# Optimization experiments

Hardware: AMD Instinct MI355X
Metric: run time of the kernel (lower is better)

## Reference

```python
import jax, jax.numpy as jnp
import numpy as np

NUM_GROUPS = 32
EPS = 1e-6


def group_norm(x, scale, bias):
    b, c, h, w = x.shape
    g = NUM_GROUPS
    xg = x.reshape(b, g, c // g, h, w)
    mean = jnp.mean(xg, axis=(2, 3, 4), keepdims=True)
    var = jnp.var(xg, axis=(2, 3, 4), keepdims=True)
    xg = (xg - mean) * jax.lax.rsqrt(var + EPS)
    x = xg.reshape(b, c, h, w)
    return x * scale[None, :, None, None] + bias[None, :, None, None]


def conv1x1(x, w, b):
    # x: [B,C,H,W], w: [Cout,Cin], b: [Cout]
    return jnp.einsum('bchw,oc->bohw', x, w) + b[None, :, None, None]


def setup_inputs() -> dict:
    key = jax.random.key(0)
    ks = jax.random.split(key, 11)
    C = 512
    B, H, W = 8, 64, 64
    s = 1.0 / np.sqrt(C)
    inp = {
        'x': jax.random.normal(ks[0], (B, C, H, W), jnp.float32),
        'gn_scale': jnp.ones((C,), jnp.float32),
        'gn_bias': jnp.zeros((C,), jnp.float32),
        'wq': jax.random.normal(ks[1], (C, C), jnp.float32) * s,
        'bq': jnp.zeros((C,), jnp.float32),
        'wk': jax.random.normal(ks[2], (C, C), jnp.float32) * s,
        'bk': jnp.zeros((C,), jnp.float32),
        'wv': jax.random.normal(ks[3], (C, C), jnp.float32) * s,
        'bv': jnp.zeros((C,), jnp.float32),
    }
    return inp


def reference(x, gn_scale, gn_bias, wq, bq, wk, bk, wv, bv):
    b, c, h, w = x.shape
    h_ = group_norm(x, gn_scale, gn_bias)
    q = conv1x1(h_, wq, bq).reshape(b, c, h * w)  # [b,c,n]
    k = conv1x1(h_, wk, bk).reshape(b, c, h * w)
    v = conv1x1(h_, wv, bv).reshape(b, c, h * w)
    scale = jnp.asarray(c, x.dtype) ** -0.5
    # attn[b,i,j] = sum_c q[b,c,i] * k[b,c,j]
    attn = jnp.einsum('bci,bcj->bij', q, k) * scale
    attn = jax.nn.softmax(attn, axis=2)  # softmax over j (keys)
    # A[b,c,i] = sum_j v[b,c,j] * attn[b,i,j]
    A = jnp.einsum('bcj,bij->bci', v, attn).reshape(b, c, h, w)
    return x + A
```

## Files before the change

kernel.cpp:

```cpp
#include <hip/hip_runtime.h>
#include <hip/hip_bf16.h>

#define B_   8
#define C_   512
#define N_   4096
#define G_   32
#define CPG  16
#define EPSV 1e-6f

typedef short s16x8 __attribute__((ext_vector_type(8)));
typedef float f32x4 __attribute__((ext_vector_type(4)));

__device__ __forceinline__ unsigned short f2bf(float f) {
    unsigned u = __builtin_bit_cast(unsigned, f);
    u += 0x7fffu + ((u >> 16) & 1u);
    return (unsigned short)(u >> 16);
}

__device__ __forceinline__ void gload_lds16(const unsigned short* g, unsigned short* l) {
    __builtin_amdgcn_global_load_lds((const __attribute__((address_space(1))) void*)g,
                                     (__attribute__((address_space(3))) void*)l, 16, 0, 0);
}

__global__ __launch_bounds__(256) void gn_stats_k(const float* __restrict__ x,
                                                  float* __restrict__ stats) {
    int blk = blockIdx.x;
    const float4* p = (const float4*)(x + (size_t)blk * (CPG * N_));
    float s = 0.f, ss = 0.f;
    for (int i = threadIdx.x; i < (CPG * N_) / 4; i += 256) {
        float4 v = p[i];
        s  += v.x + v.y + v.z + v.w;
        ss += v.x * v.x + v.y * v.y + v.z * v.z + v.w * v.w;
    }
    for (int off = 32; off > 0; off >>= 1) {
        s  += __shfl_down(s, off);
        ss += __shfl_down(ss, off);
    }
    __shared__ float r0[4], r1[4];
    int wid = threadIdx.x >> 6;
    if ((threadIdx.x & 63) == 0) { r0[wid] = s; r1[wid] = ss; }
    __syncthreads();
    if (threadIdx.x == 0) {
        s  = r0[0] + r0[1] + r0[2] + r0[3];
        ss = r1[0] + r1[1] + r1[2] + r1[3];
        const float inv = 1.0f / (CPG * N_);
        float mean = s * inv;
        float var  = ss * inv - mean * mean;
        stats[2 * blk]     = mean;
        stats[2 * blk + 1] = rsqrtf(var + EPSV);
    }
}

__global__ __launch_bounds__(256) void cvt_w_k(const float* __restrict__ wq,
                                               const float* __restrict__ wk,
                                               const float* __restrict__ wv,
                                               unsigned short* __restrict__ wbf) {
    int i = blockIdx.x * 256 + threadIdx.x;
    const int percc = C_ * C_ / 4;
    const float* src; int li;
    if (i < percc)            { src = wq; li = i; }
    else if (i < 2 * percc)   { src = wk; li = i - percc; }
    else                      { src = wv; li = i - 2 * percc; }
    float4 v = ((const float4*)src)[li];
    unsigned u0 = (unsigned)f2bf(v.x) | ((unsigned)f2bf(v.y) << 16);
    unsigned u1 = (unsigned)f2bf(v.z) | ((unsigned)f2bf(v.w) << 16);
    uint2 o; o.x = u0; o.y = u1;
    *(uint2*)&wbf[(size_t)i * 4] = o;
}

__global__ __launch_bounds__(256) void gn_apply_k(const float* __restrict__ x,
                                                  const float* __restrict__ stats,
                                                  const float* __restrict__ gsc,
                                                  const float* __restrict__ gbi,
                                                  unsigned short* __restrict__ h_t) {
    int nt = blockIdx.x, ct = blockIdx.y, b = blockIdx.z;
    int n0 = nt * 64, c0 = ct * 64;
    __shared__ unsigned short T[64][72];
    int t = threadIdx.x;
    int cl = t >> 2, ch = t & 3;
    int c = c0 + cl;
    int g = c >> 4;
    float mean = stats[(b * G_ + g) * 2];
    float rstd = stats[(b * G_ + g) * 2 + 1];
    float sc = gsc[c] * rstd;
    float bi = gbi[c] - mean * sc;
    const float* xr = x + (size_t)(b * C_ + c) * N_ + n0 + ch * 16;
    #pragma unroll
    for (int q = 0; q < 4; ++q) {
        float4 v = *(const float4*)(xr + q * 4);
        int nl = ch * 16 + q * 4;
        T[nl + 0][cl] = f2bf(fmaf(v.x, sc, bi));
        T[nl + 1][cl] = f2bf(fmaf(v.y, sc, bi));
        T[nl + 2][cl] = f2bf(fmaf(v.z, sc, bi));
        T[nl + 3][cl] = f2bf(fmaf(v.w, sc, bi));
    }
    __syncthreads();
    #pragma unroll
    for (int it = 0; it < 2; ++it) {
        int id = t + it * 256;
        int nl = id >> 3, part = id & 7;
        s16x8 val = *(const s16x8*)&T[nl][part * 8];
        *(s16x8*)&h_t[((size_t)b * N_ + n0 + nl) * C_ + c0 + part * 8] = val;
    }
}

__device__ __forceinline__ void gemm_core(const unsigned short* A, int ldA,
                                          const unsigned short* Bm, int ldB,
                                          unsigned short* Al, unsigned short* Bl,
                                          f32x4 (&acc)[4][4], int ksteps, int t) {
    int w = t >> 6, l = t & 63;
    int wm = (w >> 1) * 64, wn = (w & 1) * 64;
    int lr = l & 15, lg = l >> 4;
    int srow = w * 16 + (l >> 2);
    int sp   = (l & 3) * 8;

    #pragma unroll
    for (int it = 0; it < 2; ++it) {
        gload_lds16(&A [(size_t)(it * 64 + srow) * ldA + sp], &Al[it * 2048 + w * 512 + l * 8]);
        gload_lds16(&Bm[(size_t)(it * 64 + srow) * ldB + sp], &Bl[it * 2048 + w * 512 + l * 8]);
    }
    __syncthreads();

    int cur = 0;
    for (int s = 0; s < ksteps; ++s) {
        if (s + 1 < ksteps) {
            const unsigned short* ga = A  + (s + 1) * 32;
            const unsigned short* gb = Bm + (s + 1) * 32;
            int off = (cur ^ 1) * 4096;
            #pragma unroll
            for (int it = 0; it < 2; ++it) {
                gload_lds16(&ga[(size_t)(it * 64 + srow) * ldA + sp], &Al[off + it * 2048 + w * 512 + l * 8]);
                gload_lds16(&gb[(size_t)(it * 64 + srow) * ldB + sp], &Bl[off + it * 2048 + w * 512 + l * 8]);
            }
        }
        const unsigned short* la = Al + cur * 4096;
        const unsigned short* lb = Bl + cur * 4096;
        s16x8 a[4], b[4];
        #pragma unroll
        for (int i = 0; i < 4; ++i) a[i] = *(const s16x8*)&la[(wm + i * 16 + lr) * 32 + lg * 8];
        #pragma unroll
        for (int j = 0; j < 4; ++j) b[j] = *(const s16x8*)&lb[(wn + j * 16 + lr) * 32 + lg * 8];
        #pragma unroll
        for (int i = 0; i < 4; ++i)
            #pragma unroll
            for (int j = 0; j < 4; ++j)
                acc[i][j] = __builtin_amdgcn_mfma_f32_16x16x32_bf16(a[i], b[j], acc[i][j], 0, 0, 0);
        __syncthreads();
        cur ^= 1;
    }
}

__global__ __launch_bounds__(256, 4) void qkv_k(const unsigned short* __restrict__ h_t,
                                                const unsigned short* __restrict__ wbf,
                                                const float* __restrict__ bq,
                                                const float* __restrict__ bk,
                                                const float* __restrict__ bv,
                                                unsigned short* __restrict__ q_t,
                                                unsigned short* __restrict__ k_t,
                                                unsigned short* __restrict__ vv) {
    int which = blockIdx.z % 3;
    int b     = blockIdx.z / 3;
    int bx = blockIdx.x, by = blockIdx.y;
    const unsigned short* A;
    const unsigned short* Bm;
    unsigned short* Cm;
    const float* bias;
    int m0, n0; size_t ldc; bool biasRow;
    const unsigned short* hb = h_t + (size_t)b * N_ * C_;
    if (which < 2) {
        A = hb; Bm = wbf + (size_t)which * C_ * C_;
        Cm = (which == 0 ? q_t : k_t) + (size_t)b * N_ * C_;
        bias = (which == 0 ? bq : bk);
        m0 = bx * 128; n0 = by * 128; ldc = C_; biasRow = false;
    } else {
        A = wbf + (size_t)2 * C_ * C_; Bm = hb;
        Cm = vv + (size_t)b * C_ * N_;
        bias = bv;
        m0 = by * 128; n0 = bx * 128; ldc = N_; biasRow = true;
    }

    __shared__ char smem[35072];
    unsigned short* Al = (unsigned short*)smem;
    unsigned short* Bl = Al + 8192;
    unsigned short* El = (unsigned short*)smem;

    int t = threadIdx.x;
    int wid = t >> 6, lane = t & 63;
    int wm = (wid >> 1) * 64, wn = (wid & 1) * 64;
    int lr = lane & 15, lg = lane >> 4;

    f32x4 acc[4][4] = {};
    gemm_core(A + (size_t)m0 * C_, C_, Bm + (size_t)n0 * C_, C_, Al, Bl, acc, C_ / 32, t);

    float rb[4][4], cb[4];
    #pragma unroll
    for (int i = 0; i < 4; ++i)
        #pragma unroll
        for (int r = 0; r < 4; ++r)
            rb[i][r] = biasRow ? bias[m0 + wm + i * 16 + lg * 4 + r] : 0.f;
    #pragma unroll
    for (int j = 0; j < 4; ++j)
        cb[j] = biasRow ? 0.f : bias[n0 + wn + j * 16 + lr];

    #pragma unroll
    for (int i = 0; i < 4; ++i)
        #pragma unroll
        for (int j = 0; j < 4; ++j) {
            int col = wn + j * 16 + lr;
            #pragma unroll
            for (int r = 0; r < 4; ++r) {
                int row = wm + i * 16 + lg * 4 + r;
                El[row * 136 + col] = f2bf(acc[i][j][r] + rb[i][r] + cb[j]);
            }
        }
    __syncthreads();
    #pragma unroll
    for (int it = 0; it < 8; ++it) {
        int id = t + it * 256;
        int row = id >> 4, part = id & 15;
        *(s16x8*)&Cm[(size_t)(m0 + row) * ldc + n0 + part * 8] =
            *(const s16x8*)&El[row * 136 + part * 8];
    }
}

__global__ __launch_bounds__(512) void zeroL_k(float* __restrict__ L) {
    L[blockIdx.x * 512 + threadIdx.x] = 0.f;
}

__global__ __launch_bounds__(256, 4) void sgemm_k(const unsigned short* __restrict__ q_t,
                                                  const unsigned short* __restrict__ k_t,
                                                  unsigned short* __restrict__ Ptil,
                                                  float* __restrict__ L,
                                                  int bbase) {
    int z = blockIdx.z;
    int b = bbase + z;
    const unsigned short* A  = q_t + (size_t)b * N_ * C_;
    const unsigned short* Bm = k_t + (size_t)b * N_ * C_;
    unsigned short* Cm = Ptil + (size_t)z * N_ * N_;
    int m0 = blockIdx.y * 128, n0 = blockIdx.x * 128;

    __shared__ char smem[35072];
    unsigned short* Al = (unsigned short*)smem;
    unsigned short* Bl = Al + 8192;
    unsigned short* El = (unsigned short*)smem;

    int t = threadIdx.x;
    int wid = t >> 6, lane = t & 63;
    int wm = (wid >> 1) * 64, wn = (wid & 1) * 64;
    int lr = lane & 15, lg = lane >> 4;

    f32x4 acc[4][4] = {};
    gemm_core(A + (size_t)m0 * C_, C_, Bm + (size_t)n0 * C_, C_, Al, Bl, acc, C_ / 32, t);

    const float SCL2 = 0.06375862f;
    float rsum[4][4];
    #pragma unroll
    for (int i = 0; i < 4; ++i)
        #pragma unroll
        for (int r = 0; r < 4; ++r) rsum[i][r] = 0.f;

    #pragma unroll
    for (int i = 0; i < 4; ++i)
        #pragma unroll
        for (int j = 0; j < 4; ++j) {
            int col = wn + j * 16 + lr;
            #pragma unroll
            for (int r = 0; r < 4; ++r) {
                float p = exp2f(acc[i][j][r] * SCL2);
                rsum[i][r] += p;
                El[(wm + i * 16 + lg * 4 + r) * 136 + col] = f2bf(p);
            }
        }
    #pragma unroll
    for (int msk = 8; msk >= 1; msk >>= 1)
        #pragma unroll
        for (int i = 0; i < 4; ++i)
            #pragma unroll
            for (int r = 0; r < 4; ++r)
                rsum[i][r] += __shfl_xor(rsum[i][r], msk);
    if (lr == 0) {
        #pragma unroll
        for (int i = 0; i < 4; ++i)
            #pragma unroll
            for (int r = 0; r < 4; ++r)
                atomicAdd(&L[(size_t)b * N_ + m0 + wm + i * 16 + lg * 4 + r], rsum[i][r]);
    }
    __syncthreads();
    #pragma unroll
    for (int it = 0; it < 8; ++it) {
        int id = t + it * 256;
        int row = id >> 4, part = id & 15;
        *(s16x8*)&Cm[(size_t)(m0 + row) * N_ + n0 + part * 8] =
            *(const s16x8*)&El[row * 136 + part * 8];
    }
}

__global__ __launch_bounds__(256, 4) void pv_k(const unsigned short* __restrict__ vv,
                                               const unsigned short* __restrict__ Ptil,
                                               const float* __restrict__ L,
                                               const float* __restrict__ x,
                                               float* __restrict__ out,
                                               int bbase) {
    int z = blockIdx.z;
    int b = bbase + z;
    const unsigned short* A  = vv + (size_t)b * C_ * N_;
    const unsigned short* Bm = Ptil + (size_t)z * N_ * N_;
    int m0 = blockIdx.y * 128, n0 = blockIdx.x * 128;
    const float* xb = x + (size_t)b * C_ * N_;
    float* ob = out + (size_t)b * C_ * N_;

    __shared__ char smem[32768];
    unsigned short* Al = (unsigned short*)smem;
    unsigned short* Bl = Al + 8192;

    int t = threadIdx.x;
    int wid = t >> 6, lane = t & 63;
    int wm = (wid >> 1) * 64, wn = (wid & 1) * 64;
    int lr = lane & 15, lg = lane >> 4;

    f32x4 acc[4][4] = {};
    gemm_core(A + (size_t)m0 * N_, N_, Bm + (size_t)n0 * N_, N_, Al, Bl, acc, N_ / 32, t);

    #pragma unroll
    for (int j = 0; j < 4; ++j) {
        int col = n0 + wn + j * 16 + lr;
        float rl = 1.0f / L[(size_t)b * N_ + col];
        #pragma unroll
        for (int i = 0; i < 4; ++i) {
            #pragma unroll
            for (int r = 0; r < 4; ++r) {
                int row = m0 + wm + i * 16 + lg * 4 + r;
                size_t off = (size_t)row * N_ + col;
                ob[off] = xb[off] + acc[i][j][r] * rl;
            }
        }
    }
}

extern "C" void kernel_launch(void* const* d_in, const int* in_sizes, int n_in,
                              void* d_out, int out_size, void* d_ws, size_t ws_size,
                              hipStream_t stream) {
    const float* x   = (const float*)d_in[0];
    const float* gsc = (const float*)d_in[1];
    const float* gbi = (const float*)d_in[2];
    const float* wq  = (const float*)d_in[3];
    const float* bq  = (const float*)d_in[4];
    const float* wk  = (const float*)d_in[5];
    const float* bk  = (const float*)d_in[6];
    const float* wv  = (const float*)d_in[7];
    const float* bv  = (const float*)d_in[8];
    float* out = (float*)d_out;

    const size_t elems = (size_t)B_ * N_ * C_;
    unsigned short* q_t   = (unsigned short*)d_ws;
    unsigned short* k_t   = q_t + elems;
    unsigned short* v     = k_t + elems;
    float*          stats = (float*)(v + elems);
    unsigned short* wbf   = (unsigned short*)(stats + 2 * B_ * G_);
    float*          L     = (float*)(wbf + (size_t)3 * C_ * C_);
    unsigned short* Ptil  = (unsigned short*)(L + (size_t)B_ * N_);
    unsigned short* h_t   = (unsigned short*)d_out;

    const size_t base_bytes = (size_t)((char*)Ptil - (char*)d_ws);
    const size_t slot_bytes = (size_t)N_ * N_ * 2;
    const bool all8 = ws_size >= base_bytes + 8 * slot_bytes;

    gn_stats_k<<<B_ * G_, 256, 0, stream>>>(x, stats);
    cvt_w_k<<<(3 * C_ * C_ / 4) / 256, 256, 0, stream>>>(wq, wk, wv, wbf);
    gn_apply_k<<<dim3(N_ / 64, C_ / 64, B_), 256, 0, stream>>>(x, stats, gsc, gbi, h_t);
    qkv_k<<<dim3(32, 4, 3 * B_), 256, 0, stream>>>(h_t, wbf, bq, bk, bv, q_t, k_t, v);
    zeroL_k<<<(B_ * N_) / 512, 512, 0, stream>>>(L);
    if (all8) {
        sgemm_k<<<dim3(32, 32, 8), 256, 0, stream>>>(q_t, k_t, Ptil, L, 0);
        pv_k<<<dim3(32, 4, 8), 256, 0, stream>>>(v, Ptil, L, x, out, 0);
    } else {
        for (int p = 0; p < 4; ++p) {
            sgemm_k<<<dim3(32, 32, 2), 256, 0, stream>>>(q_t, k_t, Ptil, L, 2 * p);
            pv_k<<<dim3(32, 4, 2), 256, 0, stream>>>(v, Ptil, L, x, out, 2 * p);
        }
    }
}
```

Baseline: 714.2 us.

## Split-K the PV GEMM with atomic accumulation when workspace limits batch slots

When the workspace cannot hold all eight probability matrices, the PV kernel now splits the key dimension across blockIdx.z so each pass still launches eight z-slices. A separate kernel first copies x into the output, and each partial result is added with float atomics. A 4-slot tier is added so fewer sgemm/pv passes are needed when the workspace allows it. The aim is to fix the low block count of the old 2-batch fallback passes, at the cost of atomic traffic, an extra copy of x, and non-deterministic summation order.

```diff
diff --git a/kernel.cpp b/kernel.cpp
--- a/kernel.cpp
+++ b/kernel.cpp
@@ -102,6 +102,14 @@
         s16x8 val = *(const s16x8*)&T[nl][part * 8];
         *(s16x8*)&h_t[((size_t)b * N_ + n0 + nl) * C_ + c0 + part * 8] = val;
     }
+}
+
+__global__ __launch_bounds__(256) void copyx_k(const float* __restrict__ x,
+                                               float* __restrict__ out) {
+    const size_t total4 = (size_t)B_ * C_ * N_ / 4;
+    size_t stride = (size_t)gridDim.x * 256;
+    for (size_t i = blockIdx.x * 256 + threadIdx.x; i < total4; i += stride)
+        ((float4*)out)[i] = ((const float4*)x)[i];
 }
 
 __device__ __forceinline__ void gemm_core(const unsigned short* A, int ldA,
@@ -295,16 +303,19 @@
     }
 }
 
+template <bool ATOMIC>
 __global__ __launch_bounds__(256, 4) void pv_k(const unsigned short* __restrict__ vv,
                                                const unsigned short* __restrict__ Ptil,
                                                const float* __restrict__ L,
                                                const float* __restrict__ x,
                                                float* __restrict__ out,
-                                               int bbase) {
+                                               int bbase, int SK) {
     int z = blockIdx.z;
-    int b = bbase + z;
-    const unsigned short* A  = vv + (size_t)b * C_ * N_;
-    const unsigned short* Bm = Ptil + (size_t)z * N_ * N_;
+    int slot = z / SK, kr = z % SK;
+    int b = bbase + slot;
+    int kOff = kr * (N_ / SK);
+    const unsigned short* A  = vv + (size_t)b * C_ * N_ + kOff;
+    const unsigned short* Bm = Ptil + (size_t)slot * N_ * N_ + kOff;
     int m0 = blockIdx.y * 128, n0 = blockIdx.x * 128;
     const float* xb = x + (size_t)b * C_ * N_;
     float* ob = out + (size_t)b * C_ * N_;
@@ -319,7 +330,7 @@
     int lr = lane & 15, lg = lane >> 4;
 
     f32x4 acc[4][4] = {};
-    gemm_core(A + (size_t)m0 * N_, N_, Bm + (size_t)n0 * N_, N_, Al, Bl, acc, N_ / 32, t);
+    gemm_core(A + (size_t)m0 * N_, N_, Bm + (size_t)n0 * N_, N_, Al, Bl, acc, (N_ / SK) / 32, t);
 
     #pragma unroll
     for (int j = 0; j < 4; ++j) {
@@ -331,7 +342,8 @@
             for (int r = 0; r < 4; ++r) {
                 int row = m0 + wm + i * 16 + lg * 4 + r;
                 size_t off = (size_t)row * N_ + col;
-                ob[off] = xb[off] + acc[i][j][r] * rl;
+                if (ATOMIC) atomicAdd(&ob[off], acc[i][j][r] * rl);
+                else        ob[off] = xb[off] + acc[i][j][r] * rl;
             }
         }
     }
@@ -363,20 +375,25 @@
 
     const size_t base_bytes = (size_t)((char*)Ptil - (char*)d_ws);
     const size_t slot_bytes = (size_t)N_ * N_ * 2;
-    const bool all8 = ws_size >= base_bytes + 8 * slot_bytes;
+    int slots = 2;
+    if      (ws_size >= base_bytes + 8 * slot_bytes) slots = 8;
+    else if (ws_size >= base_bytes + 4 * slot_bytes) slots = 4;
+    const int SK = 8 / slots;
 
     gn_stats_k<<<B_ * G_, 256, 0, stream>>>(x, stats);
     cvt_w_k<<<(3 * C_ * C_ / 4) / 256, 256, 0, stream>>>(wq, wk, wv, wbf);
     gn_apply_k<<<dim3(N_ / 64, C_ / 64, B_), 256, 0, stream>>>(x, stats, gsc, gbi, h_t);
     qkv_k<<<dim3(32, 4, 3 * B_), 256, 0, stream>>>(h_t, wbf, bq, bk, bv, q_t, k_t, v);
     zeroL_k<<<(B_ * N_) / 512, 512, 0, stream>>>(L);
-    if (all8) {
+
+    if (slots == 8) {
         sgemm_k<<<dim3(32, 32, 8), 256, 0, stream>>>(q_t, k_t, Ptil, L, 0);
-        pv_k<<<dim3(32, 4, 8), 256, 0, stream>>>(v, Ptil, L, x, out, 0);
+        pv_k<false><<<dim3(32, 4, 8), 256, 0, stream>>>(v, Ptil, L, x, out, 0, 1);
     } else {
-        for (int p = 0; p < 4; ++p) {
-            sgemm_k<<<dim3(32, 32, 2), 256, 0, stream>>>(q_t, k_t, Ptil, L, 2 * p);
-            pv_k<<<dim3(32, 4, 2), 256, 0, stream>>>(v, Ptil, L, x, out, 2 * p);
-        }
-    }
-}
+        copyx_k<<<2048, 256, 0, stream>>>(x, out);
+        for (int bb = 0; bb < B_; bb += slots) {
+            sgemm_k<<<dim3(32, 32, slots), 256, 0, stream>>>(q_t, k_t, Ptil, L, bb);
+            pv_k<true><<<dim3(32, 4, 8), 256, 0, stream>>>(v, Ptil, L, x, out, bb, SK);
+        }
+    }
+}
```

Result: faster. 624.4 us (-12.6%).
